# Kernel optimization log

Measured on AMD Instinct MI355X. Metric: run time of the kernel, lower is better.

The kernel has to match this reference:

```python
import jax, jax.numpy as jnp
import numpy as np

B, S, H, E, VP, LAB, V, L = 64, 196, 512, 512, 8, 16, 10000, 32
T = L - 1
IN = E + VP + LAB + E + E  # lstm input size


def setup_inputs() -> dict:
    key = jax.random.key(0)
    ks = jax.random.split(key, 30)
    rn = lambda k, sh, s=0.02: jax.random.normal(k, sh, jnp.float32) * s
    length = jnp.concatenate([jnp.array([L], jnp.int64),
                              jax.random.randint(ks[6], (B - 1,), 2, L + 1).astype(jnp.int64)])
    return {
        "image": jax.random.normal(ks[0], (B, S, H), jnp.float32),
        "view_position": jax.random.normal(ks[1], (B, VP), jnp.float32),
        "label": jax.random.normal(ks[2], (B, LAB), jnp.float32),
        "topic": jax.random.normal(ks[3], (B, E), jnp.float32),
        "temp": jax.random.uniform(ks[4], (B, 1), jnp.float32) + 0.5,
        "emb_W": rn(ks[7], (V, E)),
        "fc_h_W": rn(ks[8], (E, H)), "fc_h_b": jnp.zeros((H,), jnp.float32),
        "fc_m_W": rn(ks[9], (E, H)), "fc_m_b": jnp.zeros((H,), jnp.float32),
        "W_ih": rn(ks[10], (IN, 4 * H)), "W_hh": rn(ks[11], (H, 4 * H)),
        "b_ih": jnp.zeros((4 * H,), jnp.float32), "b_hh": jnp.zeros((4 * H,), jnp.float32),
        "att_fc_W": rn(ks[12], (H, 2 * H)), "att_fc_b": jnp.zeros((2 * H,), jnp.float32),
        "att_v_W": rn(ks[13], (H, H)), "att_v_b": jnp.zeros((H,), jnp.float32),
        "att_hh_W": rn(ks[14], (H, H)), "att_hh_b": jnp.zeros((H,), jnp.float32),
        "att_s_W": rn(ks[15], (H, H)), "att_s_b": jnp.zeros((H,), jnp.float32),
        "att_z_W": rn(ks[16], (H, 1)), "att_z_b": jnp.zeros((1,), jnp.float32),
        "fc_p_W": rn(ks[17], (H, V)), "fc_p_b": jnp.zeros((V,), jnp.float32),
        "text": jax.random.randint(ks[5], (B, L), 0, V).astype(jnp.int64),
        "length": length,
    }


def _decode(image, view_position, label, topic, temp,
            emb_W, fc_h_W, fc_h_b, fc_m_W, fc_m_b,
            W_ih, W_hh, b_ih, b_hh,
            att_fc_W, att_fc_b, att_v_W, att_v_b, att_hh_W, att_hh_b,
            att_s_W, att_s_b, att_z_W, att_z_b, fc_p_W, fc_p_b,
            text, length):
    emb = emb_W[text]                      # (B, L, E)
    img_mean = image.mean(1)               # (B, H)
    h0 = jnp.tanh(img_mean @ fc_h_W + fc_h_b)
    m0 = jnp.tanh(img_mean @ fc_m_W + fc_m_b)
    static_x = jnp.concatenate([img_mean, view_position, label, topic], 1)  # (B, E+VP+LAB+E)
    v_proj = image @ att_v_W + att_v_b     # (B, S, H), constant across steps
    mask = (jnp.arange(T)[:, None] < (length - 1)[None, :]).astype(image.dtype)  # (T, B)
    xs = (jnp.swapaxes(emb[:, :T], 0, 1), mask)  # ((T,B,E), (T,B))

    def step(carry, inp):
        h, m = carry
        x_t, msk = inp
        x = jnp.concatenate([static_x, x_t], 1)
        gates = x @ W_ih + b_ih + h @ W_hh + b_hh
        i, f, g, o = jnp.split(gates, 4, axis=1)
        m2 = jax.nn.sigmoid(f) * m + jax.nn.sigmoid(i) * jnp.tanh(g)
        h2 = jax.nn.sigmoid(o) * jnp.tanh(m2)
        # adaptive attention
        hs = jnp.tanh(h2 @ att_fc_W + att_fc_b)         # (B, 2H)
        hh, s = hs[:, :H], hs[:, H:]
        _h = hh @ att_hh_W + att_hh_b                   # (B, H)
        _s = s @ att_s_W + att_s_b                      # (B, H)
        z_v = jnp.tanh(v_proj + _h[:, None, :])         # (B, S, H)
        z_s = jnp.tanh(_s + _h)                         # (B, H)
        z = jnp.concatenate([z_v, z_s[:, None, :]], 1)  # (B, S+1, H)
        zz = (z @ att_z_W).squeeze(-1) + att_z_b        # (B, S+1)
        a = jax.nn.softmax(zz, axis=-1)
        c = jnp.einsum('bs,bsh->bh', a[:, :S], image) + a[:, S:] * s
        logp = jax.nn.log_softmax((c + h2) @ fc_p_W + fc_p_b, axis=-1) / temp
        return (h2, m2), (a * msk[:, None], logp * msk[:, None])

    (_, _), (att, logp) = jax.lax.scan(step, (h0, m0), xs)
    return jnp.swapaxes(att, 0, 1), jnp.swapaxes(logp, 0, 1)  # (B,T,S+1), (B,T,V)


def reference(image, view_position, label, topic, temp,
              emb_W, fc_h_W, fc_h_b, fc_m_W, fc_m_b,
              W_ih, W_hh, b_ih, b_hh,
              att_fc_W, att_fc_b, att_v_W, att_v_b, att_hh_W, att_hh_b,
              att_s_W, att_s_b, att_z_W, att_z_b, fc_p_W, fc_p_b,
              text, length):
    return _decode(image, view_position, label, topic, temp,
                   emb_W, fc_h_W, fc_h_b, fc_m_W, fc_m_b,
                   W_ih, W_hh, b_ih, b_hh,
                   att_fc_W, att_fc_b, att_v_W, att_v_b, att_hh_W, att_hh_b,
                   att_s_W, att_s_b, att_z_W, att_z_b, fc_p_W, fc_p_b,
                   text, length)
```

## Files before the change

### kernel.cpp

```cpp
#include <hip/hip_runtime.h>
#include <hip/hip_bf16.h>

#define NB 64
#define NS 196
#define NH 512
#define NV 10000
#define NL 32
#define NT 31
#define NSP 197
#define LSTM_BLOCKS 32

typedef __attribute__((ext_vector_type(4))) float  f32x4;
typedef __attribute__((ext_vector_type(8))) short  short8;
typedef __attribute__((ext_vector_type(4))) short  s16x4;
typedef __attribute__((ext_vector_type(8))) __bf16 bf16x8;

__device__ __forceinline__ float sigm(float x){ return 1.0f/(1.0f+__expf(-x)); }
__device__ __forceinline__ float tanh_f(float x){ return 1.0f - 2.0f/(1.0f+__expf(2.0f*x)); }
__device__ __forceinline__ short f2bf(float f){
  unsigned u = __float_as_uint(f);
  u += 0x7FFFu + ((u>>16)&1u);
  return (short)(u>>16);
}
__device__ __forceinline__ float bf2f(short s){
  return __uint_as_float(((unsigned)(unsigned short)s)<<16);
}

#define NJOBS 10
struct TrJob { const float* src; short* dst; int K; int N; int tcols; };
struct TrJobs { TrJob j[NJOBS]; int cum[NJOBS+1]; };

__global__ __launch_bounds__(256)
void k_tr_all(TrJobs jobs)
{
  __shared__ float tsh[32][33];
  const int g = blockIdx.x;
  int ji = 0;
  #pragma unroll
  for (int i = 0; i < NJOBS; ++i) if (g >= jobs.cum[i+1]) ji = i+1;
  const TrJob J = jobs.j[ji];
  const int lt = g - jobs.cum[ji];
  const int n0 = (lt % J.tcols)*32, k0 = (lt / J.tcols)*32;
  for (int i = threadIdx.x; i < 1024; i += 256) {
    const int kl = i>>5, nl = i&31;
    if (k0+kl < J.K && n0+nl < J.N) tsh[kl][nl] = J.src[(size_t)(k0+kl)*J.N + n0+nl];
  }
  __syncthreads();
  for (int i = threadIdx.x; i < 1024; i += 256) {
    const int nl = i>>5, kl = i&31;
    if (n0+nl < J.N && k0+kl < J.K) J.dst[(size_t)(n0+nl)*J.K + k0+kl] = f2bf(tsh[kl][nl]);
  }
}

template<int ACT, int CBF, int ABF>
__global__ __launch_bounds__(256)
void mfma_gemm2(const void* __restrict__ Ap, int lda,
                const short* __restrict__ Bt, int ldb,
                const float* __restrict__ bias, const float* __restrict__ bias2,
                void* __restrict__ Cp, int ldc,
                int M, int N, int K)
{
  __shared__ short ash[128][40];
  __shared__ short bsh[128][40];
  const int bn0 = blockIdx.x*128, bm0 = blockIdx.y*128;
  const int tid = threadIdx.x;
  const int w = tid>>6, l = tid&63;
  const int wr = w>>1, wc = w&1;
  const int lrow = l&15, lk = (l>>4)*8;

  f32x4 acc[4][4];
  #pragma unroll
  for (int i=0;i<4;++i)
    #pragma unroll
    for (int j=0;j<4;++j){ f32x4 z = {0.f,0.f,0.f,0.f}; acc[i][j] = z; }

  const int srow = tid>>1, skc = (tid&1)*16;

  const int ksteps = (K+31)>>5;
  for (int ks=0; ks<ksteps; ++ks) {
    const int k0 = ks<<5;
    {
      short8 t0 = {0,0,0,0,0,0,0,0}, t1 = {0,0,0,0,0,0,0,0};
      const int gm = bm0 + srow;
      if (ABF) {
        const short* A = (const short*)Ap;
        if (gm < M) {
          if (k0+skc+16 <= K) {
            const short* src = A + (size_t)gm*lda + (k0+skc);
            t0 = *reinterpret_cast<const short8*>(src);
            t1 = *reinterpret_cast<const short8*>(src+8);
          } else {
            #pragma unroll
            for (int e=0;e<8;++e){ int gk=k0+skc+e;   if (gk<K) t0[e]=A[(size_t)gm*lda+gk]; }
            #pragma unroll
            for (int e=0;e<8;++e){ int gk=k0+skc+8+e; if (gk<K) t1[e]=A[(size_t)gm*lda+gk]; }
          }
        }
      } else {
        const float* A = (const float*)Ap;
        if (gm < M) {
          if (k0+skc+16 <= K) {
            const float* src = A + (size_t)gm*lda + (k0+skc);
            f32x4 v0 = *reinterpret_cast<const f32x4*>(src);
            f32x4 v1 = *reinterpret_cast<const f32x4*>(src+4);
            f32x4 v2 = *reinterpret_cast<const f32x4*>(src+8);
            f32x4 v3 = *reinterpret_cast<const f32x4*>(src+12);
            t0[0]=f2bf(v0.x); t0[1]=f2bf(v0.y); t0[2]=f2bf(v0.z); t0[3]=f2bf(v0.w);
            t0[4]=f2bf(v1.x); t0[5]=f2bf(v1.y); t0[6]=f2bf(v1.z); t0[7]=f2bf(v1.w);
            t1[0]=f2bf(v2.x); t1[1]=f2bf(v2.y); t1[2]=f2bf(v2.z); t1[3]=f2bf(v2.w);
            t1[4]=f2bf(v3.x); t1[5]=f2bf(v3.y); t1[6]=f2bf(v3.z); t1[7]=f2bf(v3.w);
          } else {
            #pragma unroll
            for (int e=0;e<8;++e){ int gk=k0+skc+e;   if (gk<K) t0[e]=f2bf(A[(size_t)gm*lda+gk]); }
            #pragma unroll
            for (int e=0;e<8;++e){ int gk=k0+skc+8+e; if (gk<K) t1[e]=f2bf(A[(size_t)gm*lda+gk]); }
          }
        }
      }
      *reinterpret_cast<short8*>(&ash[srow][skc])   = t0;
      *reinterpret_cast<short8*>(&ash[srow][skc+8]) = t1;
    }
    {
      short8 t0 = {0,0,0,0,0,0,0,0}, t1 = {0,0,0,0,0,0,0,0};
      const int gn = bn0 + srow;
      if (gn < N) {
        if (k0+skc+16 <= K) {
          const short* src = Bt + (size_t)gn*ldb + (k0+skc);
          t0 = *reinterpret_cast<const short8*>(src);
          t1 = *reinterpret_cast<const short8*>(src+8);
        } else {
          #pragma unroll
          for (int e=0;e<8;++e){ int gk=k0+skc+e;   if (gk<K) t0[e]=Bt[(size_t)gn*ldb+gk]; }
          #pragma unroll
          for (int e=0;e<8;++e){ int gk=k0+skc+8+e; if (gk<K) t1[e]=Bt[(size_t)gn*ldb+gk]; }
        }
      }
      *reinterpret_cast<short8*>(&bsh[srow][skc])   = t0;
      *reinterpret_cast<short8*>(&bsh[srow][skc+8]) = t1;
    }
    __syncthreads();
    short8 af[4], bfm[4];
    #pragma unroll
    for (int fm=0;fm<4;++fm) af[fm]  = *reinterpret_cast<const short8*>(&ash[wr*64+fm*16+lrow][lk]);
    #pragma unroll
    for (int fn=0;fn<4;++fn) bfm[fn] = *reinterpret_cast<const short8*>(&bsh[wc*64+fn*16+lrow][lk]);
    #pragma unroll
    for (int fm=0;fm<4;++fm)
      #pragma unroll
      for (int fn=0;fn<4;++fn)
        acc[fm][fn] = __builtin_amdgcn_mfma_f32_16x16x32_bf16(
            __builtin_bit_cast(bf16x8, af[fm]),
            __builtin_bit_cast(bf16x8, bfm[fn]),
            acc[fm][fn], 0, 0, 0);
    __syncthreads();
  }
  #pragma unroll
  for (int fm=0;fm<4;++fm){
    #pragma unroll
    for (int fn=0;fn<4;++fn){
      const int gcol = bn0 + wc*64 + fn*16 + lrow;
      if (gcol >= N) continue;
      float bv = 0.f;
      if (bias)  bv += bias[gcol];
      if (bias2) bv += bias2[gcol];
      const int grow0 = bm0 + wr*64 + fm*16 + (l>>4)*4;
      #pragma unroll
      for (int ri=0;ri<4;++ri){
        const int grow = grow0 + ri;
        if (grow >= M) continue;
        float v = acc[fm][fn][ri] + bv;
        if (ACT==1) v = tanh_f(v);
        if (CBF) reinterpret_cast<short*>(Cp)[(size_t)grow*ldc+gcol] = f2bf(v);
        else     reinterpret_cast<float*>(Cp)[(size_t)grow*ldc+gcol] = v;
      }
    }
  }
}

__global__ __launch_bounds__(256)
void k_mean_static(const float* __restrict__ image, const float* __restrict__ vp,
                   const float* __restrict__ lab, const float* __restrict__ topic,
                   float* __restrict__ imean, float* __restrict__ statx)
{
  const int b = blockIdx.y;
  const int h = blockIdx.x*256 + threadIdx.x;
  float s = 0.f;
  for (int j = 0; j < NS; ++j) s += image[((size_t)b*NS + j)*NH + h];
  const float mn = s * (1.0f/196.0f);
  imean[b*NH + h]       = mn;
  statx[b*1048 + h]     = mn;
  statx[b*1048 + 536+h] = topic[b*NH + h];
  if (blockIdx.x == 0) {
    if (threadIdx.x < 8)       statx[b*1048 + 512 + threadIdx.x]     = vp[b*8 + threadIdx.x];
    else if (threadIdx.x < 24) statx[b*1048 + 520 + (threadIdx.x-8)] = lab[b*16 + threadIdx.x-8];
  }
}

__global__ __launch_bounds__(256)
void k_gather(const float* __restrict__ embW, const int* __restrict__ text,
              short* __restrict__ X)
{
  const int r = blockIdx.x;
  const int t = r >> 6, b = r & 63;
  const int tok = text[b*NL + t];
  for (int e = threadIdx.x; e < NH; e += 256)
    X[(size_t)r*NH + e] = f2bf(embW[(size_t)tok*NH + e]);
}

__global__ __launch_bounds__(256)
void k_f2bf_vec(const float* __restrict__ s, short* __restrict__ d, int n)
{
  int i = (blockIdx.x*256 + threadIdx.x)*4;
  if (i+4 <= n) {
    f32x4 v = *reinterpret_cast<const f32x4*>(s+i);
    s16x4 o; o[0]=f2bf(v.x); o[1]=f2bf(v.y); o[2]=f2bf(v.z); o[3]=f2bf(v.w);
    *reinterpret_cast<s16x4*>(d+i) = o;
  }
}

__global__ void k_init_ctr(unsigned* c){ if (threadIdx.x==0 && blockIdx.x==0) *c = 0u; }

__global__ __launch_bounds__(256, 1)
void lstm_persist(const float* __restrict__ Gs,
                  const float* __restrict__ Ge,
                  const short* __restrict__ WhhT,
                  short* __restrict__ hbf0,
                  short* __restrict__ hbf1,
                  const float* __restrict__ m0,
                  float* __restrict__ Hout,
                  unsigned* __restrict__ ctr)
{
  __shared__ __align__(16) char smem[65536];
  float (*gshm)[64][17] = reinterpret_cast<float(*)[64][17]>(smem);
  const int bx = blockIdx.x;
  const int tid = threadIdx.x, w = tid>>6, l = tid&63;
  const int lrow = l&15, lhi = l>>4;
  const int jbase = bx*16;
  const int sw = (lrow&7)<<4;

  short8 bfrag[16];
  {
    const short* wp = WhhT + (size_t)(w*512 + jbase + lrow)*512 + lhi*8;
    #pragma unroll
    for (int ks=0; ks<16; ++ks)
      bfrag[ks] = *reinterpret_cast<const short8*>(wp + ks*32);
  }
  float gsr[16];
  #pragma unroll
  for (int fm=0; fm<4; ++fm)
    #pragma unroll
    for (int ri=0; ri<4; ++ri)
      gsr[fm*4+ri] = Gs[(size_t)(fm*16 + lhi*4 + ri)*2048 + w*512 + jbase + lrow];

  const int cb = tid>>2, cj = (tid&3)*4;
  float mreg[4];
  #pragma unroll
  for (int q=0; q<4; ++q) mreg[q] = m0[(size_t)cb*512 + jbase + cj + q];

  for (int t=0; t<NT; ++t) {
    {
      const char* hbytes = (const char*)((t&1) ? hbf1 : hbf0);
      #pragma unroll
      for (int q=0; q<16; ++q) {
        const int B = (q*256 + tid)*16;
        const int r = B >> 10;
        const int src = (r<<10) | ((B & 1023) ^ ((r&7)<<4));
        *reinterpret_cast<short8*>(smem + B) =
            *reinterpret_cast<const short8*>(hbytes + src);
      }
    }
    float ger[16];
    {
      const float* ge = Ge + (size_t)t*NB*2048;
      #pragma unroll
      for (int fm=0; fm<4; ++fm)
        #pragma unroll
        for (int ri=0; ri<4; ++ri)
          ger[fm*4+ri] = ge[(size_t)(fm*16 + lhi*4 + ri)*2048 + w*512 + jbase + lrow];
    }
    __syncthreads();

    f32x4 acc[4];
    #pragma unroll
    for (int fm=0; fm<4; ++fm){ f32x4 z = {0.f,0.f,0.f,0.f}; acc[fm] = z; }
    #pragma unroll
    for (int ks=0; ks<16; ++ks) {
      const int kb = ks*64 + lhi*16;
      #pragma unroll
      for (int fm=0; fm<4; ++fm) {
        const int r = fm*16 + lrow;
        const short8 a = *reinterpret_cast<const short8*>(smem + r*1024 + (kb ^ sw));
        acc[fm] = __builtin_amdgcn_mfma_f32_16x16x32_bf16(
            __builtin_bit_cast(bf16x8, a),
            __builtin_bit_cast(bf16x8, bfrag[ks]), acc[fm], 0, 0, 0);
      }
    }
    __syncthreads();

    #pragma unroll
    for (int fm=0; fm<4; ++fm)
      #pragma unroll
      for (int ri=0; ri<4; ++ri)
        gshm[w][fm*16 + lhi*4 + ri][lrow] = acc[fm][ri] + gsr[fm*4+ri] + ger[fm*4+ri];
    __syncthreads();

    float h2v[4];
    #pragma unroll
    for (int q=0; q<4; ++q) {
      const float gi = gshm[0][cb][cj+q];
      const float gf = gshm[1][cb][cj+q];
      const float gg = gshm[2][cb][cj+q];
      const float go = gshm[3][cb][cj+q];
      mreg[q] = sigm(gf)*mreg[q] + sigm(gi)*tanh_f(gg);
      h2v[q]  = sigm(go)*tanh_f(mreg[q]);
    }
    {
      float* ho = Hout + ((size_t)t*NB + cb)*NH + jbase + cj;
      ho[0]=h2v[0]; ho[1]=h2v[1]; ho[2]=h2v[2]; ho[3]=h2v[3];
      short* hn = ((t&1) ? hbf0 : hbf1) + (size_t)cb*512 + jbase + cj;
      hn[0]=f2bf(h2v[0]); hn[1]=f2bf(h2v[1]); hn[2]=f2bf(h2v[2]); hn[3]=f2bf(h2v[3]);
    }

    if (t != NT-1) {
      __syncthreads();
      if (tid == 0) {
        __hip_atomic_fetch_add(ctr, 1u, __ATOMIC_RELEASE, __HIP_MEMORY_SCOPE_AGENT);
        const unsigned tgt = (unsigned)LSTM_BLOCKS * (unsigned)(t+1);
        unsigned spins = 0;
        while (__hip_atomic_load(ctr, __ATOMIC_RELAXED, __HIP_MEMORY_SCOPE_AGENT) < tgt
               && ++spins < (1u<<20)) {
          __builtin_amdgcn_s_sleep(2);
        }
        (void)__hip_atomic_load(ctr, __ATOMIC_ACQUIRE, __HIP_MEMORY_SCOPE_AGENT);
      }
      __syncthreads();
    }
  }
}

__global__ __launch_bounds__(256)
void k_zs(const float* __restrict__ Hh, const float* __restrict__ Ss,
          const float* __restrict__ zw, float* __restrict__ zz)
{
  const int wid = blockIdx.x*4 + (threadIdx.x >> 6);
  const int l = threadIdx.x & 63;
  const int t = wid >> 6, b = wid & 63;
  float s = 0.f;
  #pragma unroll
  for (int j = 0; j < 8; ++j) {
    const int h = l + 64*j;
    s += tanh_f(Hh[(size_t)wid*NH + h] + Ss[(size_t)wid*NH + h]) * zw[h];
  }
  #pragma unroll
  for (int off = 1; off < 64; off <<= 1) s += __shfl_xor(s, off);
  if (l == 0) zz[((size_t)b*NT + t)*200 + 196] = s;
}

__global__ __launch_bounds__(256)
void k_att1(const short* __restrict__ vpbf, const float* __restrict__ Hh,
            const float* __restrict__ zw, float* __restrict__ zz)
{
  __shared__ short vp_sh[16][512];
  __shared__ short hh_sh[NT][512];
  __shared__ float zw_sh[512];
  const int b = blockIdx.y, s0 = blockIdx.x*16;
  for (int i = threadIdx.x; i < 1024; i += 256) {
    const int row = i >> 6, c8 = (i & 63)*8;
    const int gs = s0 + row;
    short8 v = {0,0,0,0,0,0,0,0};
    if (gs < NS) v = *reinterpret_cast<const short8*>(&vpbf[((size_t)b*NS + gs)*NH + c8]);
    *reinterpret_cast<short8*>(&vp_sh[row][c8]) = v;
  }
  for (int i = threadIdx.x; i < NT*512; i += 256) {
    const int t = i >> 9, h = i & 511;
    hh_sh[t][h] = f2bf(Hh[((size_t)t*NB + b)*NH + h]);
  }
  for (int i = threadIdx.x; i < 512; i += 256) zw_sh[i] = zw[i];
  __syncthreads();
  const int w = threadIdx.x >> 6, l = threadIdx.x & 63;
  for (int si = w; si < 16; si += 4) {
    const int gs = s0 + si;
    if (gs >= NS) continue;
    float vv[8], zv[8];
    #pragma unroll
    for (int j = 0; j < 8; ++j) {
      const int h = l + 64*j;
      vv[j] = bf2f(vp_sh[si][h]);
      zv[j] = zw_sh[h];
    }
    for (int t = 0; t < NT; ++t) {
      float acc = 0.f;
      #pragma unroll
      for (int j = 0; j < 8; ++j) {
        const int h = l + 64*j;
        acc += tanh_f(vv[j] + bf2f(hh_sh[t][h])) * zv[j];
      }
      #pragma unroll
      for (int off = 1; off < 64; off <<= 1) acc += __shfl_xor(acc, off);
      if (l == 0) zz[((size_t)b*NT + t)*200 + gs] = acc;
    }
  }
}

__global__ __launch_bounds__(256)
void k_att2(const float* __restrict__ zz, const int* __restrict__ length,
            float* __restrict__ att, float* __restrict__ abuf)
{
  __shared__ float red[4];
  const int rowm = blockIdx.x;
  const int b = rowm / NT, t = rowm % NT;
  const int tid = threadIdx.x, w = tid >> 6, l = tid & 63;
  float v = -1e30f;
  if (tid < NSP) v = zz[(size_t)rowm*200 + tid];
  float mx = v;
  #pragma unroll
  for (int off = 1; off < 64; off <<= 1) mx = fmaxf(mx, __shfl_xor(mx, off));
  if (l == 0) red[w] = mx;
  __syncthreads();
  mx = fmaxf(fmaxf(red[0], red[1]), fmaxf(red[2], red[3]));
  __syncthreads();
  float p = (tid < NSP) ? __expf(v - mx) : 0.f;
  float sm = p;
  #pragma unroll
  for (int off = 1; off < 64; off <<= 1) sm += __shfl_xor(sm, off);
  if (l == 0) red[w] = sm;
  __syncthreads();
  const float sum = red[0] + red[1] + red[2] + red[3];
  if (tid < NSP) {
    const float a = p / sum;
    abuf[(size_t)rowm*NSP + tid] = a;
    const int msk = (t < length[b] - 1);
    att[(size_t)rowm*NSP + tid] = msk ? a : 0.f;
  }
}

__global__ __launch_bounds__(256)
void k_att3(const float* __restrict__ abuf, const float* __restrict__ image,
            const float* __restrict__ HS, const float* __restrict__ H2,
            short* __restrict__ R)
{
  __shared__ float a_sh[NT][NSP];
  const int b = blockIdx.y;
  const int h = blockIdx.x*256 + threadIdx.x;
  for (int i = threadIdx.x; i < NT*NSP; i += 256)
    a_sh[i/NSP][i%NSP] = abuf[((size_t)b*NT + i/NSP)*NSP + (i%NSP)];
  __syncthreads();
  float acc[NT];
  #pragma unroll
  for (int t = 0; t < NT; ++t) acc[t] = 0.f;
  for (int s = 0; s < NS; ++s) {
    const float x = image[((size_t)b*NS + s)*NH + h];
    #pragma unroll
    for (int t = 0; t < NT; ++t) acc[t] = fmaf(a_sh[t][s], x, acc[t]);
  }
  #pragma unroll
  for (int t = 0; t < NT; ++t) {
    const size_t r = (size_t)t*NB + b;
    const float sv  = HS[r*1024 + 512 + h];
    const float h2v = H2[r*NH + h];
    R[((size_t)b*NT + t)*NH + h] = f2bf(acc[t] + a_sh[t][196]*sv + h2v);
  }
}

__global__ __launch_bounds__(256)
void k_logsm(float* __restrict__ logp, const int* __restrict__ length,
             const float* __restrict__ temp)
{
  __shared__ float red[4];
  const int row = blockIdx.x;
  const int b = row / NT, t = row % NT;
  float* p = logp + (size_t)row*NV;
  f32x4* p4 = reinterpret_cast<f32x4*>(p);
  const int tid = threadIdx.x, w = tid >> 6, l = tid & 63;
  const bool masked = !(t < length[b] - 1);
  if (masked) {
    f32x4 z = {0.f,0.f,0.f,0.f};
    for (int i = tid; i < NV/4; i += 256) p4[i] = z;
    return;
  }
  float mx = -1e30f;
  for (int i = tid; i < NV/4; i += 256) {
    f32x4 v = p4[i];
    mx = fmaxf(mx, fmaxf(fmaxf(v.x, v.y), fmaxf(v.z, v.w)));
  }
  #pragma unroll
  for (int off = 1; off < 64; off <<= 1) mx = fmaxf(mx, __shfl_xor(mx, off));
  if (l == 0) red[w] = mx;
  __syncthreads();
  mx = fmaxf(fmaxf(red[0], red[1]), fmaxf(red[2], red[3]));
  __syncthreads();
  float sm = 0.f;
  for (int i = tid; i < NV/4; i += 256) {
    f32x4 v = p4[i];
    sm += __expf(v.x - mx) + __expf(v.y - mx) + __expf(v.z - mx) + __expf(v.w - mx);
  }
  #pragma unroll
  for (int off = 1; off < 64; off <<= 1) sm += __shfl_xor(sm, off);
  if (l == 0) red[w] = sm;
  __syncthreads();
  const float lse = __logf(red[0] + red[1] + red[2] + red[3]);
  const float rt = 1.0f / temp[b];
  const float sh = mx + lse;
  for (int i = tid; i < NV/4; i += 256) {
    f32x4 v = p4[i];
    v.x = (v.x - sh)*rt; v.y = (v.y - sh)*rt; v.z = (v.z - sh)*rt; v.w = (v.w - sh)*rt;
    p4[i] = v;
  }
}

static const size_t O_STATIC = 0;
static const size_t O_IMEAN  = O_STATIC + (size_t)64*1048;
static const size_t O_H0     = O_IMEAN  + (size_t)64*512;
static const size_t O_M      = O_H0     + (size_t)64*512;
static const size_t O_GSTAT  = O_M      + (size_t)64*512;
static const size_t O_XEMB   = O_GSTAT  + (size_t)64*2048;
static const size_t O_GEMB   = O_XEMB   + (size_t)1984*256;
static const size_t O_H2     = O_GEMB   + (size_t)1984*2048;
static const size_t O_HS     = O_H2     + (size_t)1984*512;
static const size_t O_HH     = O_HS     + (size_t)1984*1024;
static const size_t O_SS     = O_HH     + (size_t)1984*512;
static const size_t O_R      = O_SS     + (size_t)1984*512;
static const size_t O_ZZ     = O_R      + (size_t)1984*256;
static const size_t O_ABUF   = O_ZZ     + (size_t)1984*200;
static const size_t O_VPBF   = O_ABUF   + (size_t)1984*197;
static const size_t O_WHHT   = O_VPBF   + (size_t)12544*256;
static const size_t O_HBF0   = O_WHHT   + (size_t)2048*256;
static const size_t O_HBF1   = O_HBF0   + (size_t)64*256;
static const size_t O_CTR    = O_HBF1   + (size_t)64*256;
static const size_t O_WTFCH  = O_CTR    + 64;
static const size_t O_WTFCM  = O_WTFCH  + (size_t)512*256;
static const size_t O_WTIHS  = O_WTFCM  + (size_t)512*256;
static const size_t O_WTIHE  = O_WTIHS  + (size_t)2048*524;
static const size_t O_WTAV   = O_WTIHE  + (size_t)2048*256;
static const size_t O_WTAFC  = O_WTAV   + (size_t)512*256;
static const size_t O_WTAHH  = O_WTAFC  + (size_t)1024*256;
static const size_t O_WTASS  = O_WTAHH  + (size_t)512*256;
static const size_t O_WTFCP  = O_WTASS  + (size_t)512*256;
static const size_t OFF_LOGP = (size_t)NB*NT*NSP;

extern "C" void kernel_launch(void* const* d_in, const int* in_sizes, int n_in,
                              void* d_out, int out_size, void* d_ws, size_t ws_size,
                              hipStream_t stream) {
  const float* image   = (const float*)d_in[0];
  const float* viewp   = (const float*)d_in[1];
  const float* label   = (const float*)d_in[2];
  const float* topic   = (const float*)d_in[3];
  const float* temp    = (const float*)d_in[4];
  const float* embW    = (const float*)d_in[5];
  const float* fc_h_W  = (const float*)d_in[6];
  const float* fc_h_b  = (const float*)d_in[7];
  const float* fc_m_W  = (const float*)d_in[8];
  const float* fc_m_b  = (const float*)d_in[9];
  const float* W_ih    = (const float*)d_in[10];
  const float* W_hh    = (const float*)d_in[11];
  const float* b_ih    = (const float*)d_in[12];
  const float* b_hh    = (const float*)d_in[13];
  const float* att_fc_W= (const float*)d_in[14];
  const float* att_fc_b= (const float*)d_in[15];
  const float* att_v_W = (const float*)d_in[16];
  const float* att_v_b = (const float*)d_in[17];
  const float* att_hh_W= (const float*)d_in[18];
  const float* att_hh_b= (const float*)d_in[19];
  const float* att_s_W = (const float*)d_in[20];
  const float* att_s_b = (const float*)d_in[21];
  const float* att_z_W = (const float*)d_in[22];
  const float* fc_p_W  = (const float*)d_in[24];
  const float* fc_p_b  = (const float*)d_in[25];
  const int*   text    = (const int*)d_in[26];
  const int*   length  = (const int*)d_in[27];

  float* ws = (float*)d_ws;
  float* out_att  = (float*)d_out;
  float* out_logp = (float*)d_out + OFF_LOGP;
  short* xemb  = (short*)(ws + O_XEMB);
  short* rbf   = (short*)(ws + O_R);
  short* vpbf  = (short*)(ws + O_VPBF);
  short* whhT  = (short*)(ws + O_WHHT);
  short* hbf0  = (short*)(ws + O_HBF0);
  short* hbf1  = (short*)(ws + O_HBF1);
  unsigned* ctr = (unsigned*)(ws + O_CTR);
  short* wtfch = (short*)(ws + O_WTFCH);
  short* wtfcm = (short*)(ws + O_WTFCM);
  short* wtihs = (short*)(ws + O_WTIHS);
  short* wtihe = (short*)(ws + O_WTIHE);
  short* wtav  = (short*)(ws + O_WTAV);
  short* wtafc = (short*)(ws + O_WTAFC);
  short* wtahh = (short*)(ws + O_WTAHH);
  short* wtass = (short*)(ws + O_WTASS);
  short* wtfcp = (short*)(ws + O_WTFCP);

  k_init_ctr<<<1, 64, 0, stream>>>(ctr);
  k_mean_static<<<dim3(2,NB), 256, 0, stream>>>(image, viewp, label, topic,
                                                ws+O_IMEAN, ws+O_STATIC);
  k_gather<<<NB*NT, 256, 0, stream>>>(embW, text, xemb);
  {
    TrJobs jobs;
    auto set = [&](int i, const float* s, short* d, int K, int N){
      jobs.j[i].src = s; jobs.j[i].dst = d; jobs.j[i].K = K; jobs.j[i].N = N;
      jobs.j[i].tcols = (N+31)/32;
    };
    set(0, fc_h_W,  wtfch, 512, 512);
    set(1, fc_m_W,  wtfcm, 512, 512);
    set(2, W_ih,    wtihs, 1048, 2048);
    set(3, W_ih + (size_t)1048*2048, wtihe, 512, 2048);
    set(4, W_hh,    whhT,  512, 2048);
    set(5, att_v_W, wtav,  512, 512);
    set(6, att_fc_W,wtafc, 512, 1024);
    set(7, att_hh_W,wtahh, 512, 512);
    set(8, att_s_W, wtass, 512, 512);
    set(9, fc_p_W,  wtfcp, 512, 10000);
    jobs.cum[0] = 0;
    for (int i = 0; i < NJOBS; ++i) {
      const int trows = (jobs.j[i].K+31)/32;
      jobs.cum[i+1] = jobs.cum[i] + trows*jobs.j[i].tcols;
    }
    k_tr_all<<<jobs.cum[NJOBS], 256, 0, stream>>>(jobs);
  }

  mfma_gemm2<1,0,0><<<dim3(4,1), 256, 0, stream>>>(ws+O_IMEAN,512, wtfch,512,
      fc_h_b,nullptr, ws+O_H0,512, 64,512,512);
  mfma_gemm2<1,0,0><<<dim3(4,1), 256, 0, stream>>>(ws+O_IMEAN,512, wtfcm,512,
      fc_m_b,nullptr, ws+O_M,512, 64,512,512);
  mfma_gemm2<0,0,0><<<dim3(16,1), 256, 0, stream>>>(ws+O_STATIC,1048, wtihs,1048,
      b_ih,b_hh, ws+O_GSTAT,2048, 64,2048,1048);
  mfma_gemm2<0,0,1><<<dim3(16,16), 256, 0, stream>>>(xemb,512, wtihe,512,
      nullptr,nullptr, ws+O_GEMB,2048, 1984,2048,512);
  mfma_gemm2<0,1,0><<<dim3(4,98), 256, 0, stream>>>(image,512, wtav,512,
      att_v_b,nullptr, vpbf,512, 12544,512,512);
  k_f2bf_vec<<<32, 256, 0, stream>>>(ws+O_H0, hbf0, NB*NH);

  lstm_persist<<<LSTM_BLOCKS, 256, 0, stream>>>(ws+O_GSTAT, ws+O_GEMB, whhT,
                                                hbf0, hbf1, ws+O_M, ws+O_H2, ctr);

  mfma_gemm2<1,0,0><<<dim3(8,16), 256, 0, stream>>>(ws+O_H2,512, wtafc,512,
      att_fc_b,nullptr, ws+O_HS,1024, 1984,1024,512);
  mfma_gemm2<0,0,0><<<dim3(4,16), 256, 0, stream>>>(ws+O_HS,1024, wtahh,512,
      att_hh_b,nullptr, ws+O_HH,512, 1984,512,512);
  mfma_gemm2<0,0,0><<<dim3(4,16), 256, 0, stream>>>(ws+O_HS+512,1024, wtass,512,
      att_s_b,nullptr, ws+O_SS,512, 1984,512,512);
  k_zs<<<NB*NT/4, 256, 0, stream>>>(ws+O_HH, ws+O_SS, att_z_W, ws+O_ZZ);
  k_att1<<<dim3(13,NB), 256, 0, stream>>>(vpbf, ws+O_HH, att_z_W, ws+O_ZZ);
  k_att2<<<NB*NT, 256, 0, stream>>>(ws+O_ZZ, length, out_att, ws+O_ABUF);
  k_att3<<<dim3(2,NB), 256, 0, stream>>>(ws+O_ABUF, image, ws+O_HS, ws+O_H2, rbf);

  mfma_gemm2<0,0,1><<<dim3(79,16), 256, 0, stream>>>(rbf,512, wtfcp,512,
      fc_p_b,nullptr, out_logp,10000, 1984,10000,512);
  k_logsm<<<NB*NT, 256, 0, stream>>>(out_logp, length, temp);
}
```

Before: 1.048 ms.

## Split persistent LSTM into 8 independent batch groups with per-group flag sync

The persistent LSTM kernel is repartitioned from 32 blocks that each own 16 hidden columns across all 64 batch rows into 64 blocks of 512 threads, arranged as 8 batch groups of 8 rows with 8 column slices of 64 each. The single global atomic counter barrier is replaced by per-group flag arrays, so each block waits only on the 8 blocks in its own batch group. The goal is to shorten the serial per-step critical path, since each block stages less h into shared memory and syncs with fewer peers. In exchange, half of each 16-row MFMA tile is padding (only 8 batch rows are real), each block holds twice as many W_hh fragments, and more blocks must be co-resident for the spin-wait to make progress.

```diff
diff --git a/kernel.cpp b/kernel.cpp
--- a/kernel.cpp
+++ b/kernel.cpp
@@ -8,7 +8,6 @@
 #define NL 32
 #define NT 31
 #define NSP 197
-#define LSTM_BLOCKS 32
 
 typedef __attribute__((ext_vector_type(4))) float  f32x4;
 typedef __attribute__((ext_vector_type(8))) short  short8;
@@ -218,120 +217,115 @@
   }
 }
 
-__global__ void k_init_ctr(unsigned* c){ if (threadIdx.x==0 && blockIdx.x==0) *c = 0u; }
-
-__global__ __launch_bounds__(256, 1)
-void lstm_persist(const float* __restrict__ Gs,
-                  const float* __restrict__ Ge,
-                  const short* __restrict__ WhhT,
-                  short* __restrict__ hbf0,
-                  short* __restrict__ hbf1,
-                  const float* __restrict__ m0,
-                  float* __restrict__ Hout,
-                  unsigned* __restrict__ ctr)
-{
-  __shared__ __align__(16) char smem[65536];
-  float (*gshm)[64][17] = reinterpret_cast<float(*)[64][17]>(smem);
-  const int bx = blockIdx.x;
-  const int tid = threadIdx.x, w = tid>>6, l = tid&63;
-  const int lrow = l&15, lhi = l>>4;
-  const int jbase = bx*16;
-  const int sw = (lrow&7)<<4;
-
-  short8 bfrag[16];
+__global__ void k_init_ctr(unsigned* c){ c[threadIdx.x] = 0u; }
+
+__global__ __launch_bounds__(512, 1)
+void lstm_persist8(const float* __restrict__ Gs,
+                   const float* __restrict__ Ge,
+                   const short* __restrict__ WhhT,
+                   short* __restrict__ hbuf0,
+                   short* __restrict__ hbuf1,
+                   const float* __restrict__ m0,
+                   float* __restrict__ Hout,
+                   unsigned* __restrict__ flags)
+{
+  __shared__ __align__(16) short hsh[16][512];
+  __shared__ float gsh[4][8][68];
+  const int gid = blockIdx.x >> 3, mid = blockIdx.x & 7;
+  const int tid = threadIdx.x;
+  const int w = tid >> 6, l = tid & 63;
+  const int lrow = l & 15, lhi = l >> 4;
+  const int gate = w & 3, chalf = w >> 2;
+  const int cb = mid*64 + chalf*32;
+
+  short8 bfrag[2][16];
+  #pragma unroll
+  for (int nf=0; nf<2; ++nf) {
+    const short* wp = WhhT + (size_t)(gate*512 + cb + nf*16 + lrow)*512 + lhi*8;
+    #pragma unroll
+    for (int ks=0; ks<16; ++ks)
+      bfrag[nf][ks] = *reinterpret_cast<const short8*>(wp + ks*32);
+  }
+
+  const int brow = tid >> 6;
+  const int ccol = tid & 63;
+  const int gb = gid*8 + brow;
+  const int gj = mid*64 + ccol;
+  float mreg = m0[(size_t)gb*NH + gj];
+  float gs4[4];
+  #pragma unroll
+  for (int g=0; g<4; ++g) gs4[g] = Gs[(size_t)gb*2048 + g*512 + gj];
+
   {
-    const short* wp = WhhT + (size_t)(w*512 + jbase + lrow)*512 + lhi*8;
-    #pragma unroll
-    for (int ks=0; ks<16; ++ks)
-      bfrag[ks] = *reinterpret_cast<const short8*>(wp + ks*32);
-  }
-  float gsr[16];
-  #pragma unroll
-  for (int fm=0; fm<4; ++fm)
-    #pragma unroll
-    for (int ri=0; ri<4; ++ri)
-      gsr[fm*4+ri] = Gs[(size_t)(fm*16 + lhi*4 + ri)*2048 + w*512 + jbase + lrow];
-
-  const int cb = tid>>2, cj = (tid&3)*4;
-  float mreg[4];
-  #pragma unroll
-  for (int q=0; q<4; ++q) mreg[q] = m0[(size_t)cb*512 + jbase + cj + q];
+    short8 z = {0,0,0,0,0,0,0,0};
+    *reinterpret_cast<short8*>((char*)&hsh[0][0] + (8 + (tid>>6))*1024 + (tid&63)*16) = z;
+  }
+
+  const int srow = tid >> 6, sc = (tid & 63)*16;
+  const int swS = (srow&7)<<4;
+  const unsigned ftgt_base = gid*32;
 
   for (int t=0; t<NT; ++t) {
     {
-      const char* hbytes = (const char*)((t&1) ? hbf1 : hbf0);
+      const char* hb = (const char*)((t&1) ? hbuf1 : hbuf0);
+      short8 v = *reinterpret_cast<const short8*>(hb + ((size_t)(gid*8+srow)*512)*2 + sc);
+      *reinterpret_cast<short8*>((char*)&hsh[0][0] + srow*1024 + (sc ^ swS)) = v;
+    }
+    float ge4[4];
+    {
+      const float* gep = Ge + (size_t)t*NB*2048 + (size_t)gb*2048 + gj;
       #pragma unroll
-      for (int q=0; q<16; ++q) {
-        const int B = (q*256 + tid)*16;
-        const int r = B >> 10;
-        const int src = (r<<10) | ((B & 1023) ^ ((r&7)<<4));
-        *reinterpret_cast<short8*>(smem + B) =
-            *reinterpret_cast<const short8*>(hbytes + src);
-      }
-    }
-    float ger[16];
-    {
-      const float* ge = Ge + (size_t)t*NB*2048;
-      #pragma unroll
-      for (int fm=0; fm<4; ++fm)
-        #pragma unroll
-        for (int ri=0; ri<4; ++ri)
-          ger[fm*4+ri] = ge[(size_t)(fm*16 + lhi*4 + ri)*2048 + w*512 + jbase + lrow];
+      for (int g=0; g<4; ++g) ge4[g] = gep[g*512];
     }
     __syncthreads();
 
-    f32x4 acc[4];
-    #pragma unroll
-    for (int fm=0; fm<4; ++fm){ f32x4 z = {0.f,0.f,0.f,0.f}; acc[fm] = z; }
+    f32x4 acc0 = {0.f,0.f,0.f,0.f}, acc1 = {0.f,0.f,0.f,0.f};
     #pragma unroll
     for (int ks=0; ks<16; ++ks) {
       const int kb = ks*64 + lhi*16;
-      #pragma unroll
-      for (int fm=0; fm<4; ++fm) {
-        const int r = fm*16 + lrow;
-        const short8 a = *reinterpret_cast<const short8*>(smem + r*1024 + (kb ^ sw));
-        acc[fm] = __builtin_amdgcn_mfma_f32_16x16x32_bf16(
-            __builtin_bit_cast(bf16x8, a),
-            __builtin_bit_cast(bf16x8, bfrag[ks]), acc[fm], 0, 0, 0);
+      const short8 a = *reinterpret_cast<const short8*>(
+          (char*)&hsh[0][0] + lrow*1024 + (kb ^ ((lrow&7)<<4)));
+      acc0 = __builtin_amdgcn_mfma_f32_16x16x32_bf16(
+          __builtin_bit_cast(bf16x8, a), __builtin_bit_cast(bf16x8, bfrag[0][ks]), acc0, 0,0,0);
+      acc1 = __builtin_amdgcn_mfma_f32_16x16x32_bf16(
+          __builtin_bit_cast(bf16x8, a), __builtin_bit_cast(bf16x8, bfrag[1][ks]), acc1, 0,0,0);
+    }
+    #pragma unroll
+    for (int ri=0; ri<4; ++ri) {
+      const int row = lhi*4 + ri;
+      if (row < 8) {
+        gsh[gate][row][chalf*32 + lrow]      = acc0[ri];
+        gsh[gate][row][chalf*32 + 16 + lrow] = acc1[ri];
       }
     }
     __syncthreads();
 
-    #pragma unroll
-    for (int fm=0; fm<4; ++fm)
-      #pragma unroll
-      for (int ri=0; ri<4; ++ri)
-        gshm[w][fm*16 + lhi*4 + ri][lrow] = acc[fm][ri] + gsr[fm*4+ri] + ger[fm*4+ri];
-    __syncthreads();
-
-    float h2v[4];
-    #pragma unroll
-    for (int q=0; q<4; ++q) {
-      const float gi = gshm[0][cb][cj+q];
-      const float gf = gshm[1][cb][cj+q];
-      const float gg = gshm[2][cb][cj+q];
-      const float go = gshm[3][cb][cj+q];
-      mreg[q] = sigm(gf)*mreg[q] + sigm(gi)*tanh_f(gg);
-      h2v[q]  = sigm(go)*tanh_f(mreg[q]);
-    }
-    {
-      float* ho = Hout + ((size_t)t*NB + cb)*NH + jbase + cj;
-      ho[0]=h2v[0]; ho[1]=h2v[1]; ho[2]=h2v[2]; ho[3]=h2v[3];
-      short* hn = ((t&1) ? hbf0 : hbf1) + (size_t)cb*512 + jbase + cj;
-      hn[0]=f2bf(h2v[0]); hn[1]=f2bf(h2v[1]); hn[2]=f2bf(h2v[2]); hn[3]=f2bf(h2v[3]);
-    }
+    const float gi = gsh[0][brow][ccol] + gs4[0] + ge4[0];
+    const float gf = gsh[1][brow][ccol] + gs4[1] + ge4[1];
+    const float gg = gsh[2][brow][ccol] + gs4[2] + ge4[2];
+    const float go = gsh[3][brow][ccol] + gs4[3] + ge4[3];
+    mreg = sigm(gf)*mreg + sigm(gi)*tanh_f(gg);
+    const float h2 = sigm(go)*tanh_f(mreg);
+    Hout[((size_t)t*NB + gb)*NH + gj] = h2;
+    *(((t&1) ? hbuf0 : hbuf1) + (size_t)gb*512 + gj) = f2bf(h2);
 
     if (t != NT-1) {
       __syncthreads();
-      if (tid == 0) {
-        __hip_atomic_fetch_add(ctr, 1u, __ATOMIC_RELEASE, __HIP_MEMORY_SCOPE_AGENT);
-        const unsigned tgt = (unsigned)LSTM_BLOCKS * (unsigned)(t+1);
+      if (tid == 0)
+        __hip_atomic_store(&flags[ftgt_base + mid], (unsigned)(t+1),
+                           __ATOMIC_RELEASE, __HIP_MEMORY_SCOPE_AGENT);
+      if (tid < 64) {
+        const unsigned tgt = (unsigned)(t+1);
         unsigned spins = 0;
-        while (__hip_atomic_load(ctr, __ATOMIC_RELAXED, __HIP_MEMORY_SCOPE_AGENT) < tgt
-               && ++spins < (1u<<20)) {
-          __builtin_amdgcn_s_sleep(2);
+        for (;;) {
+          unsigned f = tgt;
+          if (l < 8) f = __hip_atomic_load(&flags[ftgt_base + l],
+                                           __ATOMIC_RELAXED, __HIP_MEMORY_SCOPE_AGENT);
+          if (__all(f >= tgt) || ++spins >= (1u<<20)) break;
+          __builtin_amdgcn_s_sleep(1);
         }
-        (void)__hip_atomic_load(ctr, __ATOMIC_ACQUIRE, __HIP_MEMORY_SCOPE_AGENT);
+        (void)__hip_atomic_load(&flags[ftgt_base],
+                                __ATOMIC_ACQUIRE, __HIP_MEMORY_SCOPE_AGENT);
       }
       __syncthreads();
     }
@@ -527,7 +521,7 @@
 static const size_t O_HBF0   = O_WHHT   + (size_t)2048*256;
 static const size_t O_HBF1   = O_HBF0   + (size_t)64*256;
 static const size_t O_CTR    = O_HBF1   + (size_t)64*256;
-static const size_t O_WTFCH  = O_CTR    + 64;
+static const size_t O_WTFCH  = O_CTR    + 256;
 static const size_t O_WTFCM  = O_WTFCH  + (size_t)512*256;
 static const size_t O_WTIHS  = O_WTFCM  + (size_t)512*256;
 static const size_t O_WTIHE  = O_WTIHS  + (size_t)2048*524;
@@ -589,7 +583,7 @@
   short* wtass = (short*)(ws + O_WTASS);
   short* wtfcp = (short*)(ws + O_WTFCP);
 
-  k_init_ctr<<<1, 64, 0, stream>>>(ctr);
+  k_init_ctr<<<1, 256, 0, stream>>>(ctr);
   k_mean_static<<<dim3(2,NB), 256, 0, stream>>>(image, viewp, label, topic,
                                                 ws+O_IMEAN, ws+O_STATIC);
   k_gather<<<NB*NT, 256, 0, stream>>>(embW, text, xemb);
@@ -629,8 +623,8 @@
       att_v_b,nullptr, vpbf,512, 12544,512,512);
   k_f2bf_vec<<<32, 256, 0, stream>>>(ws+O_H0, hbf0, NB*NH);
 
-  lstm_persist<<<LSTM_BLOCKS, 256, 0, stream>>>(ws+O_GSTAT, ws+O_GEMB, whhT,
-                                                hbf0, hbf1, ws+O_M, ws+O_H2, ctr);
+  lstm_persist8<<<64, 512, 0, stream>>>(ws+O_GSTAT, ws+O_GEMB, whhT,
+                                        hbf0, hbf1, ws+O_M, ws+O_H2, ctr);
 
   mfma_gemm2<1,0,0><<<dim3(8,16), 256, 0, stream>>>(ws+O_H2,512, wtafc,512,
       att_fc_b,nullptr, ws+O_HS,1024, 1984,1024,512);
```

Result: faster. 846.2 us (-19.2%).
